# Optimization experiments

Hardware: AMD Instinct MI355X
Metric: run time of the kernel (lower is better)

## Reference

```python
import jax, jax.numpy as jnp
import numpy as np

B, E, N, D = 32, 16384, 1000, 128


def setup_inputs() -> dict:
    key = jax.random.key(0)
    ks = jax.random.split(key, 8)
    s = 1.0 / np.sqrt(D)
    return {
        "edge_attr": jax.random.normal(ks[0], (B, E, D), dtype=jnp.float32),
        "edge_index": jax.random.randint(ks[1], (B, 2, E), 0, N, dtype=jnp.int32),
        "W1": jax.random.uniform(ks[2], (D, D), jnp.float32, -s, s),
        "b1": jax.random.uniform(ks[3], (D,), jnp.float32, -s, s),
        "W2": jax.random.uniform(ks[4], (D, D), jnp.float32, -s, s),
        "b2": jax.random.uniform(ks[5], (D,), jnp.float32, -s, s),
        "Wo": jax.random.uniform(ks[6], (1, D), jnp.float32, -s, s),
        "bo": jax.random.uniform(ks[7], (1,), jnp.float32, -s, s),
    }


def reference(edge_attr, edge_index, W1, b1, W2, b2, Wo, bo):
    # MLP over edge features: two hidden silu layers then sigmoid output * 10
    h = jax.nn.silu(jnp.einsum("bed,kd->bek", edge_attr, W1) + b1)
    h = jax.nn.silu(jnp.einsum("bed,kd->bek", h, W2) + b2)
    vals = jax.nn.sigmoid(jnp.einsum("bed,kd->bek", h, Wo) + bo)[..., 0] * 10.0  # [B, E]

    src = edge_index[:, 0, :]  # [B, E]
    dst = edge_index[:, 1, :]  # [B, E]
    b_idx = jnp.arange(B, dtype=edge_index.dtype)[:, None]  # [B, 1]
    heat = jnp.zeros((B, N, N), dtype=edge_attr.dtype).at[b_idx, src, dst].set(vals)

    # undirected_graph=True: symmetrize
    return (heat + jnp.swapaxes(heat, 1, 2)) * 0.5
```

## Files before the change

kernel.cpp:

```cpp
#include <hip/hip_runtime.h>
#include <hip/hip_bf16.h>
#include <math.h>

#define B_ 32
#define E_ 16384
#define N_ 1000
#define D_ 128
#define NN_ (N_ * N_)
#define T_ 8

typedef __attribute__((ext_vector_type(8))) short bf16x8;
typedef __attribute__((ext_vector_type(4))) float f32x4;

__device__ __forceinline__ unsigned short f2bf(float f) {
    unsigned u = __float_as_uint(f);
    u += 0x7FFFu + ((u >> 16) & 1u);
    return (unsigned short)(u >> 16);
}

__device__ __forceinline__ unsigned pk2(float lo, float hi) {
    __hip_bfloat162 h = __float22bfloat162_rn(make_float2(lo, hi));
    return *(unsigned*)&h;
}

__device__ __forceinline__ f32x4 mfma16(bf16x8 a, bf16x8 b, f32x4 c) {
    return __builtin_amdgcn_mfma_f32_16x16x32_bf16(a, b, c, 0, 0, 0);
}

__device__ __forceinline__ float silu_(float z) {
    return z * __builtin_amdgcn_rcpf(1.0f + __expf(-z));
}

__device__ __forceinline__ float dec17(unsigned x) {
    return (float)((x & 0x1FFFFu) - 1u) * (10.0f / 131070.0f);
}

__device__ __forceinline__ void gload_lds16(const void* g, void* l) {
    __builtin_amdgcn_global_load_lds(
        (const __attribute__((address_space(1))) unsigned*)g,
        (__attribute__((address_space(3))) unsigned*)l, 16, 0, 0);
}

__global__ void prep_weights(const float* __restrict__ W1,
                             const float* __restrict__ W2,
                             unsigned short* __restrict__ wsz) {
    int t = blockIdx.x * 256 + threadIdx.x;
    int w = t >> 14, e = t & 16383;
    int row = e >> 7, pos = e & 127;
    int src_col = pos;
    if (w) {
        int q = pos >> 5, gg = (pos >> 3) & 3, nn = (pos >> 2) & 1, r = pos & 3;
        src_col = (q * 2 + nn) * 16 + gg * 4 + r;
    }
    float v = (w ? W2 : W1)[row * 128 + src_col];
    char* dst = (char*)wsz + (size_t)w * 32768 + row * 256 + ((pos * 2) ^ ((row & 7) << 4));
    *(unsigned short*)dst = f2bf(v);
}

__global__ __launch_bounds__(512, 2) void mlp_scatter_kernel(
    const float* __restrict__ X, const int* __restrict__ EI,
    const unsigned short* __restrict__ wsz,
    const float* __restrict__ b1, const float* __restrict__ b2,
    const float* __restrict__ Wo, const float* __restrict__ bo,
    unsigned* __restrict__ out)
{
    __shared__ __align__(16) char Wb[65536];
    __shared__ __align__(16) float BiasL[384];

    const int tid = threadIdx.x;
    const int lane = tid & 63;
    const int wv = tid >> 6;
    const int l15 = lane & 15;
    const int g = (lane >> 4) & 3;

    const int bb = blockIdx.x >> 4;
    const int e0 = (blockIdx.x & 15) * (128 * T_);

    if (tid < 96) {
        const float* src = tid < 32 ? b1 : (tid < 64 ? b2 : Wo);
        ((f32x4*)BiasL)[tid] = ((const f32x4*)src)[tid & 31];
    }
    const float bo0 = bo[0];

    #pragma unroll
    for (int it = 0; it < 8; ++it) {
        int off = it * 8192 + tid * 16;
        gload_lds16((const char*)wsz + off, Wb + off);
    }
    __syncthreads();

    #pragma unroll 1
    for (int st = 0; st < T_; ++st) {
        const int eb0 = e0 + st * 128 + wv * 16;

        const int eis = EI[(size_t)bb * 2 * E_ + eb0 + l15];
        const int eid = EI[(size_t)bb * 2 * E_ + E_ + eb0 + l15];

        bf16x8 a[4];
        {
            const float* p0 = X + ((size_t)bb * E_ + eb0 + l15) * D_ + g * 8;
            #pragma unroll
            for (int ks = 0; ks < 4; ++ks) {
                float4 u0 = *(const float4*)(p0 + ks * 32);
                float4 u1 = *(const float4*)(p0 + ks * 32 + 4);
                bf16x8 t; unsigned* tu = (unsigned*)&t;
                tu[0] = pk2(u0.x, u0.y); tu[1] = pk2(u0.z, u0.w);
                tu[2] = pk2(u1.x, u1.y); tu[3] = pk2(u1.z, u1.w);
                a[ks] = t;
            }
        }

        bf16x8 pa[4];
        #pragma unroll
        for (int q = 0; q < 4; ++q) {
            f32x4 acc1[2];
            acc1[0] = (f32x4){0.f, 0.f, 0.f, 0.f};
            acc1[1] = (f32x4){0.f, 0.f, 0.f, 0.f};

            #pragma unroll
            for (int ks = 0; ks < 4; ++ks)
                #pragma unroll
                for (int nn = 0; nn < 2; ++nn) {
                    int row = l15 + (q * 2 + nn) * 16;
                    bf16x8 aw = *(const bf16x8*)(Wb + row * 256 +
                                  ((ks * 64 + g * 16) ^ ((row & 7) << 4)));
                    acc1[nn] = mfma16(aw, a[ks], acc1[nn]);
                }

            f32x4 b1q0 = ((f32x4*)BiasL)[(q * 2 + 0) * 4 + g];
            f32x4 b1q1 = ((f32x4*)BiasL)[(q * 2 + 1) * 4 + g];
            unsigned* au = (unsigned*)&pa[q];
            au[0] = pk2(silu_(acc1[0][0] + b1q0[0]), silu_(acc1[0][1] + b1q0[1]));
            au[1] = pk2(silu_(acc1[0][2] + b1q0[2]), silu_(acc1[0][3] + b1q0[3]));
            au[2] = pk2(silu_(acc1[1][0] + b1q1[0]), silu_(acc1[1][1] + b1q1[1]));
            au[3] = pk2(silu_(acc1[1][2] + b1q1[2]), silu_(acc1[1][3] + b1q1[3]));
            __builtin_amdgcn_sched_barrier(0);
        }

        f32x4 acc2[8];
        #pragma unroll
        for (int n = 0; n < 8; ++n)
            acc2[n] = (f32x4){0.f, 0.f, 0.f, 0.f};

        #pragma unroll
        for (int q = 0; q < 4; ++q) {
            #pragma unroll
            for (int n = 0; n < 8; ++n) {
                int row = l15 + n * 16;
                bf16x8 w2 = *(const bf16x8*)(Wb + 32768 + row * 256 +
                              ((q * 64 + g * 16) ^ ((row & 7) << 4)));
                acc2[n] = mfma16(w2, pa[q], acc2[n]);
            }
            __builtin_amdgcn_sched_barrier(0);
        }

        float zed = 0.f;
        #pragma unroll
        for (int n = 0; n < 8; ++n) {
            f32x4 b2q = ((f32x4*)BiasL)[32 + n * 4 + g];
            f32x4 woq = ((f32x4*)BiasL)[64 + n * 4 + g];
            zed += silu_(acc2[n][0] + b2q[0]) * woq[0];
            zed += silu_(acc2[n][1] + b2q[1]) * woq[1];
            zed += silu_(acc2[n][2] + b2q[2]) * woq[2];
            zed += silu_(acc2[n][3] + b2q[3]) * woq[3];
        }
        zed += __shfl_xor(zed, 16, 64);
        zed += __shfl_xor(zed, 32, 64);

        if (g == 0) {
            int e = eb0 + l15;
            float z = zed + bo0;
            float val = 10.0f * __builtin_amdgcn_rcpf(1.0f + __expf(-z));
            unsigned qv = (unsigned)(val * 13107.0f + 0.5f) + 1u;
            if (qv > 0x1FFFFu) qv = 0x1FFFFu;
            unsigned packed = 0x80000000u | ((unsigned)e << 17) | qv;
            atomicMax(out + ((size_t)bb * NN_ + (size_t)eis * N_ + eid), packed);
        }
    }
}

__global__ __launch_bounds__(256) void finalize_fused(
    const int* __restrict__ EI, unsigned* __restrict__ out)
{
    int i = blockIdx.x * 256 + threadIdx.x;
    int b = i >> 14, e = i & 16383;
    int s = EI[(size_t)b * 2 * E_ + e];
    int d = EI[(size_t)b * 2 * E_ + E_ + e];
    unsigned* ob = out + (size_t)b * NN_;
    unsigned x1 = ob[(size_t)s * N_ + d];
    unsigned x2 = ob[(size_t)d * N_ + s];
    float v;
    if (!(x1 >> 31) && x1)      v = __uint_as_float(x1);
    else if (!(x2 >> 31) && x2) v = __uint_as_float(x2);
    else {
        float c1 = (x1 >> 31) ? dec17(x1) : 0.0f;
        float c2 = (x2 >> 31) ? dec17(x2) : 0.0f;
        v = 0.5f * (c1 + c2);
    }
    unsigned uv = __float_as_uint(v);
    ob[(size_t)s * N_ + d] = uv;
    ob[(size_t)d * N_ + s] = uv;
}

extern "C" void kernel_launch(void* const* d_in, const int* in_sizes, int n_in,
                              void* d_out, int out_size, void* d_ws, size_t ws_size,
                              hipStream_t stream) {
    const float* X  = (const float*)d_in[0];
    const int*   EI = (const int*)d_in[1];
    const float* W1 = (const float*)d_in[2];
    const float* b1 = (const float*)d_in[3];
    const float* W2 = (const float*)d_in[4];
    const float* b2 = (const float*)d_in[5];
    const float* Wo = (const float*)d_in[6];
    const float* bo = (const float*)d_in[7];
    unsigned* out = (unsigned*)d_out;
    unsigned short* wsz = (unsigned short*)d_ws;

    prep_weights<<<dim3(128), dim3(256), 0, stream>>>(W1, W2, wsz);
    hipMemsetAsync(d_out, 0, (size_t)B_ * NN_ * sizeof(float), stream);
    mlp_scatter_kernel<<<dim3((B_ * E_) / (128 * T_)), dim3(512), 0, stream>>>(
        X, EI, wsz, b1, b2, Wo, bo, out);
    finalize_fused<<<dim3((B_ * E_) / 256), dim3(256), 0, stream>>>(EI, out);
}
```

Measured before the change: 143.9 us.

## Fuse output zero-fill into MLP kernel and split scatter into separate pass

Removes the separate memset of the 128MB output by having the MLP kernel zero-fill it with 16-byte stores, interleaved with its compute. Because the fill and the scatter can no longer be ordered inside one kernel, the MLP now writes per-edge values to workspace and a new scatter kernel does the packed atomicMax afterward. The aim is to overlap the bandwidth-bound zero fill with the MFMA work. It adds a kernel launch and an extra round trip through workspace for the edge values.

```diff
diff --git a/kernel.cpp b/kernel.cpp
--- a/kernel.cpp
+++ b/kernel.cpp
@@ -8,6 +8,7 @@
 #define D_ 128
 #define NN_ (N_ * N_)
 #define T_ 8
+#define OUT_U4 8000000
 
 typedef __attribute__((ext_vector_type(8))) short bf16x8;
 typedef __attribute__((ext_vector_type(4))) float f32x4;
@@ -57,15 +58,15 @@
     *(unsigned short*)dst = f2bf(v);
 }
 
-__global__ __launch_bounds__(512, 2) void mlp_scatter_kernel(
-    const float* __restrict__ X, const int* __restrict__ EI,
+__global__ __launch_bounds__(512, 2) void mlp_fill_kernel(
+    const float* __restrict__ X,
     const unsigned short* __restrict__ wsz,
     const float* __restrict__ b1, const float* __restrict__ b2,
     const float* __restrict__ Wo, const float* __restrict__ bo,
-    unsigned* __restrict__ out)
+    float* __restrict__ ev, uint4* __restrict__ outfill)
 {
     __shared__ __align__(16) char Wb[65536];
-    __shared__ __align__(16) float BiasL[384];
+    __shared__ __align__(16) float BiasL[388];
 
     const int tid = threadIdx.x;
     const int lane = tid & 63;
@@ -80,21 +81,22 @@
         const float* src = tid < 32 ? b1 : (tid < 64 ? b2 : Wo);
         ((f32x4*)BiasL)[tid] = ((const f32x4*)src)[tid & 31];
     }
-    const float bo0 = bo[0];
+    if (tid == 96) BiasL[384] = bo[0];
 
     #pragma unroll
     for (int it = 0; it < 8; ++it) {
         int off = it * 8192 + tid * 16;
-        gload_lds16((const char*)wsz + off, Wb + off);
+        gload_lds16((const char*)wsz + off, (char*)Wb + off);
     }
     __syncthreads();
+    const float bo0 = BiasL[384];
+
+    const uint4 z4 = make_uint4(0u, 0u, 0u, 0u);
+    const int fillbase = blockIdx.x * 512 + tid;
 
     #pragma unroll 1
     for (int st = 0; st < T_; ++st) {
         const int eb0 = e0 + st * 128 + wv * 16;
-
-        const int eis = EI[(size_t)bb * 2 * E_ + eb0 + l15];
-        const int eid = EI[(size_t)bb * 2 * E_ + E_ + eb0 + l15];
 
         bf16x8 a[4];
         {
@@ -110,6 +112,12 @@
             }
         }
 
+        #pragma unroll
+        for (int i = 0; i < 4; ++i) {
+            int idx = (st * 4 + i) * 262144 + fillbase;
+            if (idx < OUT_U4) outfill[idx] = z4;
+        }
+
         bf16x8 pa[4];
         #pragma unroll
         for (int q = 0; q < 4; ++q) {
@@ -168,15 +176,26 @@
         zed += __shfl_xor(zed, 32, 64);
 
         if (g == 0) {
-            int e = eb0 + l15;
             float z = zed + bo0;
-            float val = 10.0f * __builtin_amdgcn_rcpf(1.0f + __expf(-z));
-            unsigned qv = (unsigned)(val * 13107.0f + 0.5f) + 1u;
-            if (qv > 0x1FFFFu) qv = 0x1FFFFu;
-            unsigned packed = 0x80000000u | ((unsigned)e << 17) | qv;
-            atomicMax(out + ((size_t)bb * NN_ + (size_t)eis * N_ + eid), packed);
-        }
-    }
+            ev[(size_t)bb * E_ + eb0 + l15] =
+                10.0f * __builtin_amdgcn_rcpf(1.0f + __expf(-z));
+        }
+    }
+}
+
+__global__ __launch_bounds__(256) void scatter_packed(
+    const int* __restrict__ EI, const float* __restrict__ ev,
+    unsigned* __restrict__ out)
+{
+    int i = blockIdx.x * 256 + threadIdx.x;
+    int b = i >> 14, e = i & 16383;
+    int s = EI[(size_t)b * 2 * E_ + e];
+    int d = EI[(size_t)b * 2 * E_ + E_ + e];
+    float val = ev[i];
+    unsigned qv = (unsigned)(val * 13107.0f + 0.5f) + 1u;
+    if (qv > 0x1FFFFu) qv = 0x1FFFFu;
+    unsigned packed = 0x80000000u | ((unsigned)e << 17) | qv;
+    atomicMax(out + ((size_t)b * NN_ + (size_t)s * N_ + d), packed);
 }
 
 __global__ __launch_bounds__(256) void finalize_fused(
@@ -215,10 +234,11 @@
     const float* bo = (const float*)d_in[7];
     unsigned* out = (unsigned*)d_out;
     unsigned short* wsz = (unsigned short*)d_ws;
+    float* ev = (float*)((char*)d_ws + 65536);
 
     prep_weights<<<dim3(128), dim3(256), 0, stream>>>(W1, W2, wsz);
-    hipMemsetAsync(d_out, 0, (size_t)B_ * NN_ * sizeof(float), stream);
-    mlp_scatter_kernel<<<dim3((B_ * E_) / (128 * T_)), dim3(512), 0, stream>>>(
-        X, EI, wsz, b1, b2, Wo, bo, out);
+    mlp_fill_kernel<<<dim3((B_ * E_) / (128 * T_)), dim3(512), 0, stream>>>(
+        X, wsz, b1, b2, Wo, bo, ev, (uint4*)d_out);
+    scatter_packed<<<dim3((B_ * E_) / 256), dim3(256), 0, stream>>>(EI, ev, out);
     finalize_fused<<<dim3((B_ * E_) / 256), dim3(256), 0, stream>>>(EI, out);
 }
```

Result: slower. 148.3 us (+3.0%).
